# Kernel tuning notes

Hardware: AMD Instinct MI355X
Metric: run time of the kernel (lower is better)

## Reference

```python
import jax, jax.numpy as jnp
import numpy as np

N = 8192   # number of queries
D = 384    # MiniLM-L3 embedding dim
M = 1024   # number of unique docs (segments)


def setup_inputs() -> dict:
    key = jax.random.key(0)
    k1, k2, k3 = jax.random.split(key, 3)
    emb_q = jax.random.normal(k1, (N, D), dtype=jnp.float32)
    label = jax.random.uniform(k2, (N,), dtype=jnp.float32)  # relevance labels, >0 so group sums are nonzero
    doc_ids = jax.random.randint(k3, (N,), 0, M)              # plays the role of unique(emb_k) inverse indices
    return {"emb_q": emb_q, "label": label, "doc_ids": doc_ids}


def reference(emb_q, label, doc_ids):
    # cosine-similarity matrix between queries
    norm_q = emb_q / jnp.linalg.norm(emb_q, axis=1, keepdims=True)   # [N, D]
    sim = norm_q @ norm_q.T                                          # [N_i, N_q]

    # Original double python loop computes, for each doc group j and each row i:
    #   theta[i, q in group j] = sum_{q' in j} label[q'] * sim[i, q'] / sum_{q' in j} label[q']
    # which is a segment-sum over the column axis grouped by doc, then a gather back.
    weighted = sim * label[None, :]                                  # [N_i, N_q]
    num = jax.ops.segment_sum(weighted.T, doc_ids, num_segments=M)   # [M, N_i]
    den = jax.ops.segment_sum(label, doc_ids, num_segments=M)        # [M]
    theta = (num[doc_ids] / den[doc_ids][:, None]).T                 # [N_i, N_q]
    return theta
```

## Files before the change

kernel.cpp:

```cpp
#include <hip/hip_runtime.h>

#define N_Q   8192
#define DIM   384
#define N_DOC 1024

typedef unsigned short ushort_t;
typedef __attribute__((ext_vector_type(8))) short bf16x8;
typedef __attribute__((ext_vector_type(4))) float f32x4;

__device__ __forceinline__ float bf2f(ushort_t u) {
    union { unsigned i; float f; } c; c.i = ((unsigned)u) << 16; return c.f;
}
__device__ __forceinline__ ushort_t f2bf(float f) {
    union { float f; unsigned u; } c; c.f = f;
    unsigned r = c.u + 0x7FFF + ((c.u >> 16) & 1);
    return (ushort_t)(r >> 16);
}
__device__ __forceinline__ void gload_lds16(const void* g, void* l) {
    __builtin_amdgcn_global_load_lds((const __attribute__((address_space(1))) void*)g,
                                     (__attribute__((address_space(3))) void*)l, 16, 0, 0);
}

__global__ __launch_bounds__(256) void k_normalize(const float* __restrict__ emb,
                                                   ushort_t* __restrict__ nqb) {
    int w    = (blockIdx.x * 256 + threadIdx.x) >> 6;
    int lane = threadIdx.x & 63;
    const float* row = emb + (size_t)w * DIM;
    float v[6];
    float ss = 0.f;
#pragma unroll
    for (int r = 0; r < 6; ++r) { v[r] = row[lane + 64 * r]; ss += v[r] * v[r]; }
#pragma unroll
    for (int off = 32; off; off >>= 1) ss += __shfl_xor(ss, off);
    float inv = rsqrtf(ss);
    ushort_t* o = nqb + (size_t)w * DIM;
#pragma unroll
    for (int r = 0; r < 6; ++r) o[lane + 64 * r] = f2bf(v[r] * inv);
}

#define SS_WAVES 8
__global__ __launch_bounds__(512) void k_segsum(const ushort_t* __restrict__ nqb,
                                                const float* __restrict__ label,
                                                const int*   __restrict__ ids,
                                                ushort_t* __restrict__ Hb) {
    __shared__ float pacc[SS_WAVES][DIM];
    __shared__ float pden[SS_WAVES];
    int j    = blockIdx.x;
    int lane = threadIdx.x & 63;
    int w    = threadIdx.x >> 6;
    const int span = N_Q / SS_WAVES;
    int q0 = w * span;

    float acc[6] = {0.f, 0.f, 0.f, 0.f, 0.f, 0.f};
    float den = 0.f;

    int idc = ids[q0 + lane];
    for (int base = q0; base < q0 + span; base += 64) {
        int nb = base + 64;
        int idn = (nb < q0 + span) ? ids[nb + lane] : -1;
        unsigned long long mask = __ballot(idc == j);
        while (mask) {
            int b = __builtin_ctzll(mask);
            mask &= mask - 1;
            int q = base + b;
            float lab = label[q];
            const ushort_t* r = nqb + (size_t)q * DIM;
#pragma unroll
            for (int t = 0; t < 6; ++t) acc[t] = fmaf(lab, bf2f(r[lane + 64 * t]), acc[t]);
            den += lab;
        }
        idc = idn;
    }
#pragma unroll
    for (int t = 0; t < 6; ++t) pacc[w][lane + 64 * t] = acc[t];
    if (lane == 0) pden[w] = den;
    __syncthreads();

    int d = threadIdx.x;
    if (d < DIM) {
        float s = 0.f, dn = 0.f;
#pragma unroll
        for (int ww = 0; ww < SS_WAVES; ++ww) { s += pacc[ww][d]; dn += pden[ww]; }
        float invd = (dn > 0.f) ? (1.f / dn) : 0.f;
        Hb[(size_t)j * DIM + d] = f2bf(s * invd);
    }
}

#define BM 128
#define BN 128
#define BK 64

__global__ __launch_bounds__(256) void k_gemm(const ushort_t* __restrict__ A,
                                              const ushort_t* __restrict__ B,
                                              float* __restrict__ T) {
    __shared__ ushort_t As[BM * BK];
    __shared__ ushort_t Bs[BN * BK];
    int tid  = threadIdx.x;
    int lane = tid & 63, wid = tid >> 6;
    int wr = wid >> 1, wc = wid & 1;
    int row0 = blockIdx.y * BM, col0 = blockIdx.x * BN;
    int fr = lane & 15, kg = lane >> 4;

    f32x4 acc[4][4];
#pragma unroll
    for (int i = 0; i < 4; ++i)
#pragma unroll
        for (int j = 0; j < 4; ++j) acc[i][j] = (f32x4)0.f;

    for (int k0 = 0; k0 < DIM; k0 += BK) {
#pragma unroll
        for (int r = 0; r < 4; ++r) {
            int flat = r * 256 + tid;
            int row = flat >> 3, gd = flat & 7;
            int gs = gd ^ (row & 7);
            int wbase = (r * 256 + wid * 64) * 8;
            gload_lds16(A + (size_t)(row0 + row) * DIM + k0 + gs * 8, &As[wbase]);
            gload_lds16(B + (size_t)(col0 + row) * DIM + k0 + gs * 8, &Bs[wbase]);
        }
        __syncthreads();

#pragma unroll
        for (int ks = 0; ks < 2; ++ks) {
            bf16x8 a[4], b[4];
#pragma unroll
            for (int mi = 0; mi < 4; ++mi) {
                int m = wr * 64 + mi * 16 + fr;
                a[mi] = *(const bf16x8*)&As[m * 64 + (((ks * 4 + kg) ^ (m & 7)) << 3)];
            }
#pragma unroll
            for (int ni = 0; ni < 4; ++ni) {
                int n = wc * 64 + ni * 16 + fr;
                b[ni] = *(const bf16x8*)&Bs[n * 64 + (((ks * 4 + kg) ^ (n & 7)) << 3)];
            }
#pragma unroll
            for (int mi = 0; mi < 4; ++mi)
#pragma unroll
                for (int ni = 0; ni < 4; ++ni)
                    acc[mi][ni] = __builtin_amdgcn_mfma_f32_16x16x32_bf16(a[mi], b[ni], acc[mi][ni], 0, 0, 0);
        }
        __syncthreads();
    }

#pragma unroll
    for (int mi = 0; mi < 4; ++mi)
#pragma unroll
        for (int ni = 0; ni < 4; ++ni)
#pragma unroll
            for (int r = 0; r < 4; ++r)
                T[(size_t)(row0 + wr * 64 + mi * 16 + kg * 4 + r) * N_DOC
                  + col0 + wc * 64 + ni * 16 + fr] = acc[mi][ni][r];
}

__global__ __launch_bounds__(256) void k_expand(const float* __restrict__ T,
                                                const int*   __restrict__ ids,
                                                float* __restrict__ out) {
    __shared__ float trow[2][N_DOC];
    int i0 = blockIdx.x * 2;
    const float4* Tv = (const float4*)(T + (size_t)i0 * N_DOC);
    ((float4*)trow[0])[threadIdx.x]       = Tv[threadIdx.x];
    ((float4*)trow[0])[threadIdx.x + 256] = Tv[threadIdx.x + 256];
    __syncthreads();
    float* o0 = out + (size_t)i0 * N_Q;
    float* o1 = o0 + N_Q;
    const int4* id4 = (const int4*)ids;
#pragma unroll
    for (int it = 0; it < N_Q / 4 / 256; ++it) {
        int q4 = it * 256 + threadIdx.x;
        int4 id = id4[q4];
        ((float4*)o0)[q4] = make_float4(trow[0][id.x], trow[0][id.y], trow[0][id.z], trow[0][id.w]);
        ((float4*)o1)[q4] = make_float4(trow[1][id.x], trow[1][id.y], trow[1][id.z], trow[1][id.w]);
    }
}

extern "C" void kernel_launch(void* const* d_in, const int* in_sizes, int n_in,
                              void* d_out, int out_size, void* d_ws, size_t ws_size,
                              hipStream_t stream) {
    const float* emb   = (const float*)d_in[0];
    const float* label = (const float*)d_in[1];
    const int*   ids   = (const int*)d_in[2];
    float* out = (float*)d_out;

    ushort_t* nqb = (ushort_t*)d_ws;
    ushort_t* Hb  = nqb + (size_t)N_Q * DIM;
    float*    T   = (float*)(Hb + (size_t)N_DOC * DIM);

    k_normalize<<<N_Q / 4, 256, 0, stream>>>(emb, nqb);
    k_segsum<<<N_DOC, 512, 0, stream>>>(nqb, label, ids, Hb);
    k_gemm<<<dim3(N_DOC / BN, N_Q / BM), 256, 0, stream>>>(nqb, Hb, T);
    k_expand<<<N_Q / 2, 256, 0, stream>>>(T, ids, out);
}
```

Measured before the change: 81.73 us.

## Fuse GEMM and gather-expand into one kernel using an LDS slab

Replaces the separate tiled GEMM (which wrote an 8192x1024 fp32 T matrix) and the expand kernel with one fused kernel. Each block computes 16 query rows against all 1024 docs with MFMA, loading operands straight from global memory into registers with one-step prefetch. It stores the result in a 64KB LDS slab and then gathers by doc id to write the output directly. This removes the T round trip through global memory and one launch. In exchange there is no LDS staging for B, so every block rereads the whole doc matrix from global/L2, and register pressure is high.

```diff
diff --git a/kernel.cpp b/kernel.cpp
--- a/kernel.cpp
+++ b/kernel.cpp
@@ -15,10 +15,6 @@
     union { float f; unsigned u; } c; c.f = f;
     unsigned r = c.u + 0x7FFF + ((c.u >> 16) & 1);
     return (ushort_t)(r >> 16);
-}
-__device__ __forceinline__ void gload_lds16(const void* g, void* l) {
-    __builtin_amdgcn_global_load_lds((const __attribute__((address_space(1))) void*)g,
-                                     (__attribute__((address_space(3))) void*)l, 16, 0, 0);
 }
 
 __global__ __launch_bounds__(256) void k_normalize(const float* __restrict__ emb,
@@ -86,89 +82,66 @@
     }
 }
 
-#define BM 128
-#define BN 128
-#define BK 64
+#define FROWS 16
+__global__ __launch_bounds__(256, 2) void k_fused(const ushort_t* __restrict__ A,
+                                                  const ushort_t* __restrict__ B,
+                                                  const int*      __restrict__ ids,
+                                                  float*          __restrict__ out) {
+    __shared__ float slab[FROWS][N_DOC];
+    int tid  = threadIdx.x;
+    int lane = tid & 63, w = tid >> 6;
+    int fr = lane & 15, kg = lane >> 4;
+    int row0 = blockIdx.x * FROWS;
 
-__global__ __launch_bounds__(256) void k_gemm(const ushort_t* __restrict__ A,
-                                              const ushort_t* __restrict__ B,
-                                              float* __restrict__ T) {
-    __shared__ ushort_t As[BM * BK];
-    __shared__ ushort_t Bs[BN * BK];
-    int tid  = threadIdx.x;
-    int lane = tid & 63, wid = tid >> 6;
-    int wr = wid >> 1, wc = wid & 1;
-    int row0 = blockIdx.y * BM, col0 = blockIdx.x * BN;
-    int fr = lane & 15, kg = lane >> 4;
+    const ushort_t* Ap = A + (size_t)(row0 + fr) * DIM + kg * 8;
+    const ushort_t* Bp = B + (size_t)(w * 256 + fr) * DIM + kg * 8;
 
-    f32x4 acc[4][4];
+    f32x4 acc[16];
 #pragma unroll
-    for (int i = 0; i < 4; ++i)
+    for (int ni = 0; ni < 16; ++ni) acc[ni] = (f32x4)0.f;
+
+    bf16x8 a_c = *(const bf16x8*)Ap;
+    bf16x8 b_c[16];
 #pragma unroll
-        for (int j = 0; j < 4; ++j) acc[i][j] = (f32x4)0.f;
-
-    for (int k0 = 0; k0 < DIM; k0 += BK) {
-#pragma unroll
-        for (int r = 0; r < 4; ++r) {
-            int flat = r * 256 + tid;
-            int row = flat >> 3, gd = flat & 7;
-            int gs = gd ^ (row & 7);
-            int wbase = (r * 256 + wid * 64) * 8;
-            gload_lds16(A + (size_t)(row0 + row) * DIM + k0 + gs * 8, &As[wbase]);
-            gload_lds16(B + (size_t)(col0 + row) * DIM + k0 + gs * 8, &Bs[wbase]);
-        }
-        __syncthreads();
+    for (int ni = 0; ni < 16; ++ni) b_c[ni] = *(const bf16x8*)(Bp + (size_t)ni * 16 * DIM);
 
 #pragma unroll
-        for (int ks = 0; ks < 2; ++ks) {
-            bf16x8 a[4], b[4];
+    for (int k0 = 0; k0 < DIM; k0 += 32) {
+        bf16x8 a_n, b_n[16];
+        if (k0 + 32 < DIM) {
+            a_n = *(const bf16x8*)(Ap + k0 + 32);
 #pragma unroll
-            for (int mi = 0; mi < 4; ++mi) {
-                int m = wr * 64 + mi * 16 + fr;
-                a[mi] = *(const bf16x8*)&As[m * 64 + (((ks * 4 + kg) ^ (m & 7)) << 3)];
-            }
+            for (int ni = 0; ni < 16; ++ni)
+                b_n[ni] = *(const bf16x8*)(Bp + (size_t)ni * 16 * DIM + k0 + 32);
+        }
 #pragma unroll
-            for (int ni = 0; ni < 4; ++ni) {
-                int n = wc * 64 + ni * 16 + fr;
-                b[ni] = *(const bf16x8*)&Bs[n * 64 + (((ks * 4 + kg) ^ (n & 7)) << 3)];
-            }
+        for (int ni = 0; ni < 16; ++ni)
+            acc[ni] = __builtin_amdgcn_mfma_f32_16x16x32_bf16(a_c, b_c[ni], acc[ni], 0, 0, 0);
+        a_c = a_n;
 #pragma unroll
-            for (int mi = 0; mi < 4; ++mi)
-#pragma unroll
-                for (int ni = 0; ni < 4; ++ni)
-                    acc[mi][ni] = __builtin_amdgcn_mfma_f32_16x16x32_bf16(a[mi], b[ni], acc[mi][ni], 0, 0, 0);
-        }
-        __syncthreads();
+        for (int ni = 0; ni < 16; ++ni) b_c[ni] = b_n[ni];
     }
 
-#pragma unroll
-    for (int mi = 0; mi < 4; ++mi)
-#pragma unroll
-        for (int ni = 0; ni < 4; ++ni)
-#pragma unroll
-            for (int r = 0; r < 4; ++r)
-                T[(size_t)(row0 + wr * 64 + mi * 16 + kg * 4 + r) * N_DOC
-                  + col0 + wc * 64 + ni * 16 + fr] = acc[mi][ni][r];
-}
-
-__global__ __launch_bounds__(256) void k_expand(const float* __restrict__ T,
-                                                const int*   __restrict__ ids,
-                                                float* __restrict__ out) {
-    __shared__ float trow[2][N_DOC];
-    int i0 = blockIdx.x * 2;
-    const float4* Tv = (const float4*)(T + (size_t)i0 * N_DOC);
-    ((float4*)trow[0])[threadIdx.x]       = Tv[threadIdx.x];
-    ((float4*)trow[0])[threadIdx.x + 256] = Tv[threadIdx.x + 256];
-    __syncthreads();
-    float* o0 = out + (size_t)i0 * N_Q;
-    float* o1 = o0 + N_Q;
+    int4 idv[N_Q / 4 / 256];
     const int4* id4 = (const int4*)ids;
 #pragma unroll
+    for (int it = 0; it < N_Q / 4 / 256; ++it) idv[it] = id4[it * 256 + tid];
+
+#pragma unroll
+    for (int ni = 0; ni < 16; ++ni)
+#pragma unroll
+        for (int r = 0; r < 4; ++r)
+            slab[kg * 4 + r][w * 256 + ni * 16 + fr] = acc[ni][r];
+    __syncthreads();
+
+#pragma unroll
     for (int it = 0; it < N_Q / 4 / 256; ++it) {
-        int q4 = it * 256 + threadIdx.x;
-        int4 id = id4[q4];
-        ((float4*)o0)[q4] = make_float4(trow[0][id.x], trow[0][id.y], trow[0][id.z], trow[0][id.w]);
-        ((float4*)o1)[q4] = make_float4(trow[1][id.x], trow[1][id.y], trow[1][id.z], trow[1][id.w]);
+        int q4 = it * 256 + tid;
+        int4 id = idv[it];
+#pragma unroll
+        for (int r = 0; r < FROWS; ++r)
+            ((float4*)(out + (size_t)(row0 + r) * N_Q))[q4] =
+                make_float4(slab[r][id.x], slab[r][id.y], slab[r][id.z], slab[r][id.w]);
     }
 }
 
@@ -182,10 +155,8 @@
 
     ushort_t* nqb = (ushort_t*)d_ws;
     ushort_t* Hb  = nqb + (size_t)N_Q * DIM;
-    float*    T   = (float*)(Hb + (size_t)N_DOC * DIM);
 
     k_normalize<<<N_Q / 4, 256, 0, stream>>>(emb, nqb);
     k_segsum<<<N_DOC, 512, 0, stream>>>(nqb, label, ids, Hb);
-    k_gemm<<<dim3(N_DOC / BN, N_Q / BM), 256, 0, stream>>>(nqb, Hb, T);
-    k_expand<<<N_Q / 2, 256, 0, stream>>>(T, ids, out);
+    k_fused<<<N_Q / FROWS, 256, 0, stream>>>(nqb, Hb, ids, out);
 }
```

Result: slower. 100.8 us (+23.4%).

## Store GEMM result as bf16 and expand eight rows per block with streaming stores

Applied to the files above, without the earlier changes.

The intermediate row-by-doc matrix T is now written as bf16 instead of fp32, which halves its write and read traffic between the GEMM and expand kernels. The expand kernel now handles eight rows per block. Each thread loads its doc ids into registers once and reuses them across those rows, and the large output is written with nontemporal stores. The cost is extra rounding from holding T in bf16, which could break tight accuracy tolerances, and a larger LDS footprint per block in expand.

```diff
diff --git a/kernel.cpp b/kernel.cpp
--- a/kernel.cpp
+++ b/kernel.cpp
@@ -7,6 +7,7 @@
 typedef unsigned short ushort_t;
 typedef __attribute__((ext_vector_type(8))) short bf16x8;
 typedef __attribute__((ext_vector_type(4))) float f32x4;
+typedef __attribute__((ext_vector_type(4))) int i32x4;
 
 __device__ __forceinline__ float bf2f(ushort_t u) {
     union { unsigned i; float f; } c; c.i = ((unsigned)u) << 16; return c.f;
@@ -92,7 +93,7 @@
 
 __global__ __launch_bounds__(256) void k_gemm(const ushort_t* __restrict__ A,
                                               const ushort_t* __restrict__ B,
-                                              float* __restrict__ T) {
+                                              ushort_t* __restrict__ Tb) {
     __shared__ ushort_t As[BM * BK];
     __shared__ ushort_t Bs[BN * BK];
     int tid  = threadIdx.x;
@@ -147,28 +148,45 @@
         for (int ni = 0; ni < 4; ++ni)
 #pragma unroll
             for (int r = 0; r < 4; ++r)
-                T[(size_t)(row0 + wr * 64 + mi * 16 + kg * 4 + r) * N_DOC
-                  + col0 + wc * 64 + ni * 16 + fr] = acc[mi][ni][r];
-}
-
-__global__ __launch_bounds__(256) void k_expand(const float* __restrict__ T,
-                                                const int*   __restrict__ ids,
-                                                float* __restrict__ out) {
-    __shared__ float trow[2][N_DOC];
-    int i0 = blockIdx.x * 2;
-    const float4* Tv = (const float4*)(T + (size_t)i0 * N_DOC);
-    ((float4*)trow[0])[threadIdx.x]       = Tv[threadIdx.x];
-    ((float4*)trow[0])[threadIdx.x + 256] = Tv[threadIdx.x + 256];
+                Tb[(size_t)(row0 + wr * 64 + mi * 16 + kg * 4 + r) * N_DOC
+                   + col0 + wc * 64 + ni * 16 + fr] = f2bf(acc[mi][ni][r]);
+}
+
+#define EROWS 8
+__global__ __launch_bounds__(256) void k_expand(const ushort_t* __restrict__ Tb,
+                                                const int*      __restrict__ ids,
+                                                float*          __restrict__ out) {
+    __shared__ float trow[EROWS * N_DOC];
+    int tid = threadIdx.x;
+    int i0  = blockIdx.x * EROWS;
+
+    i32x4 idv[N_Q / 4 / 256];
+    const i32x4* id4 = (const i32x4*)ids;
+#pragma unroll
+    for (int it = 0; it < N_Q / 4 / 256; ++it) idv[it] = id4[it * 256 + tid];
+
+    const bf16x8* Tv = (const bf16x8*)(Tb + (size_t)i0 * N_DOC);
+#pragma unroll
+    for (int c = 0; c < 4; ++c) {
+        int chunk = c * 256 + tid;
+        bf16x8 v = Tv[chunk];
+        f32x4 lo = { bf2f((ushort_t)v[0]), bf2f((ushort_t)v[1]), bf2f((ushort_t)v[2]), bf2f((ushort_t)v[3]) };
+        f32x4 hi = { bf2f((ushort_t)v[4]), bf2f((ushort_t)v[5]), bf2f((ushort_t)v[6]), bf2f((ushort_t)v[7]) };
+        *(f32x4*)&trow[chunk * 8]     = lo;
+        *(f32x4*)&trow[chunk * 8 + 4] = hi;
+    }
     __syncthreads();
-    float* o0 = out + (size_t)i0 * N_Q;
-    float* o1 = o0 + N_Q;
-    const int4* id4 = (const int4*)ids;
+
 #pragma unroll
     for (int it = 0; it < N_Q / 4 / 256; ++it) {
-        int q4 = it * 256 + threadIdx.x;
-        int4 id = id4[q4];
-        ((float4*)o0)[q4] = make_float4(trow[0][id.x], trow[0][id.y], trow[0][id.z], trow[0][id.w]);
-        ((float4*)o1)[q4] = make_float4(trow[1][id.x], trow[1][id.y], trow[1][id.z], trow[1][id.w]);
+        int q4 = it * 256 + tid;
+        i32x4 id = idv[it];
+#pragma unroll
+        for (int r = 0; r < EROWS; ++r) {
+            const float* tr = &trow[r * N_DOC];
+            f32x4 v = { tr[id.x], tr[id.y], tr[id.z], tr[id.w] };
+            __builtin_nontemporal_store(v, (f32x4*)(out + (size_t)(i0 + r) * N_Q) + q4);
+        }
     }
 }
 
@@ -182,10 +200,10 @@
 
     ushort_t* nqb = (ushort_t*)d_ws;
     ushort_t* Hb  = nqb + (size_t)N_Q * DIM;
-    float*    T   = (float*)(Hb + (size_t)N_DOC * DIM);
+    ushort_t* Tb  = Hb + (size_t)N_DOC * DIM;
 
     k_normalize<<<N_Q / 4, 256, 0, stream>>>(emb, nqb);
     k_segsum<<<N_DOC, 512, 0, stream>>>(nqb, label, ids, Hb);
-    k_gemm<<<dim3(N_DOC / BN, N_Q / BM), 256, 0, stream>>>(nqb, Hb, T);
-    k_expand<<<N_Q / 2, 256, 0, stream>>>(T, ids, out);
-}
+    k_gemm<<<dim3(N_DOC / BN, N_Q / BM), 256, 0, stream>>>(nqb, Hb, Tb);
+    k_expand<<<N_Q / EROWS, 256, 0, stream>>>(Tb, ids, out);
+}
```

Measured after the change: 78.99 us. -3.4%, faster.
